# Performance work log

Hardware: AMD Instinct MI355X
Metric: run time of the kernel (lower is better)

The kernel has to match this reference:

```python
import jax, jax.numpy as jnp
import numpy as np

WEIGHT_STD = 0.1
WEIGHT_STD2 = 2.0 * WEIGHT_STD ** 2  # 0.02
CONF_THRESH = 0.9


def setup_inputs() -> dict:
    key = jax.random.key(0)
    k0, k1, k2, k3 = jax.random.split(key, 4)
    B, N, V, J = 1, 32768, 10475, 55
    # skinning weights: nonnegative, rows sum to 1 (as in SMPL-X)
    lbs_weights = jax.random.uniform(k0, (V, J), dtype=jnp.float32)
    lbs_weights = lbs_weights / jnp.sum(lbs_weights, -1, keepdims=True)
    verts_transform = jax.random.normal(k1, (B, V, 4, 4), dtype=jnp.float32)
    points = jax.random.normal(k2, (B, N, 3), dtype=jnp.float32)
    template_points = jax.random.normal(k3, (B, V, 3), dtype=jnp.float32)
    return {
        "lbs_weights": lbs_weights,
        "verts_transform": verts_transform,
        "points": points,
        "template_points": template_points,
        "K": 6,
    }


def _knn(points, template_points, K):
    """Brute-force KNN; squared L2 dists like pytorch3d knn_points. -> dists, idx [B,N,K] ascending."""
    p2 = jnp.sum(points * points, -1)[:, :, None]            # [B,N,1]
    t2 = jnp.sum(template_points * template_points, -1)[:, None, :]  # [B,1,V]
    cross = jnp.einsum("bnd,bvd->bnv", points, template_points)     # [B,N,V]
    d2 = jnp.maximum(p2 + t2 - 2.0 * cross, 0.0)
    neg_d, idx = jax.lax.top_k(-d2, K)  # largest of -d2 == smallest d2, sorted ascending
    return -neg_d, idx


def reference(lbs_weights, verts_transform, points, template_points, K):
    B = points.shape[0]
    neighbs_dist, neighbs = _knn(points, template_points, K)  # [B,N,K]

    # gather skinning weights of the K neighbors: [B,N,K,J]
    w_n = lbs_weights[neighbs]
    # confidence: neighbors whose lbs weights agree with the nearest one
    conf = jnp.exp(-jnp.sum(jnp.abs(w_n - w_n[..., 0:1, :]), -1) / WEIGHT_STD2)
    conf = (conf > CONF_THRESH).astype(neighbs_dist.dtype)
    w = jnp.exp(-neighbs_dist) * conf
    w = w / jnp.sum(w, -1, keepdims=True)  # [B,N,K]; k=0 conf always 1 -> sum > 0

    # gather per-vertex 4x4 transforms: [B,N,K,4,4]
    vt_n = verts_transform[jnp.arange(B)[:, None, None], neighbs]
    xyz_transform = jnp.sum(w[..., None, None] * vt_n, axis=2)   # [B,N,4,4]
    xyz_dist = jnp.sum(w * neighbs_dist, axis=2, keepdims=True)  # [B,N,1]
    return xyz_dist, xyz_transform
```

## Files before the change

### kernel.cpp

```cpp
#include <hip/hip_runtime.h>
#include <math.h>

#pragma clang fp contract(off)

#define NPTS  32768
#define NV    10475
#define JW    55
#define TILE  512
#define NT    21
#define NINIT 10
#define BLOCK 256
#define R     4
#define PPB   16
#define CAP   64
#define FINF  3.4e38f
#define GMARG 0.001f

#define FOR4(M) M(0) M(1) M(2) M(3)

#define LTL(dd, vv, D, I) ((dd) < (D) || ((dd) == (D) && (vv) < (I)))
#define INSL6(dd, vv, D0,I0,D1,I1,D2,I2,D3,I3,D4,I4,D5,I5) \
  if (LTL(dd, vv, D5, I5)) { \
    if (LTL(dd, vv, D4, I4)) { D5=D4; I5=I4; \
      if (LTL(dd, vv, D3, I3)) { D4=D3; I4=I3; \
        if (LTL(dd, vv, D2, I2)) { D3=D2; I3=I2; \
          if (LTL(dd, vv, D1, I1)) { D2=D1; I2=I1; \
            if (LTL(dd, vv, D0, I0)) { D1=D0; I1=I0; D0=(dd); I0=(vv); } \
            else { D1=(dd); I1=(vv); } \
          } else { D2=(dd); I2=(vv); } \
        } else { D3=(dd); I3=(vv); } \
      } else { D4=(dd); I4=(vv); } \
    } else { D5=(dd); I5=(vv); } \
  }

__global__ __launch_bounds__(BLOCK, 6)
void scarf_knn_lbs(const float* __restrict__ lbs,
                   const float* __restrict__ vtf,
                   const float* __restrict__ pts,
                   const float* __restrict__ tpl,
                   float* __restrict__ out_dist,
                   float* __restrict__ out_tf)
{
    __shared__ float4 s_tile[2][TILE];
    __shared__ float  s_bd[PPB][CAP];
    __shared__ int    s_bi[PPB][CAP];
    __shared__ int    s_cnt[PPB];
    __shared__ float  s_td[PPB][6];
    __shared__ int    s_ti[PPB][6];

    const int tid = threadIdx.x;
    const int h   = tid & 63;
    const int w   = tid >> 6;
    const int lp  = w * R;
    const int p0  = blockIdx.x * PPB + lp;

    if (tid < PPB) s_cnt[tid] = 0;

    #define DECLP(r) \
      const float Px##r = 2.0f * pts[(p0+(r))*3+0]; \
      const float Py##r = 2.0f * pts[(p0+(r))*3+1]; \
      const float Pz##r = 2.0f * pts[(p0+(r))*3+2]; \
      const float q##r  = (Px##r*Px##r + Py##r*Py##r) + Pz##r*Pz##r;
    FOR4(DECLP)

    float gx[2], gy[2], gz[2];
    #define STAGE_ISSUE(t_) { \
      _Pragma("unroll") \
      for (int k = 0; k < 2; ++k) { \
        const int j = (t_) * TILE + k * BLOCK + tid; \
        if (j < NV) { gx[k] = tpl[j*3+0]; gy[k] = tpl[j*3+1]; gz[k] = tpl[j*3+2]; } \
        else        { gx[k] = 1.0e6f;    gy[k] = 1.0e6f;    gz[k] = 1.0e6f;    } } }
    #define STAGE_WRITE(dst_) { \
      _Pragma("unroll") \
      for (int k = 0; k < 2; ++k) { \
        const float X = gx[k]+gx[k], Y = gy[k]+gy[k], Z = gz[k]+gz[k]; \
        s_tile[dst_][k * BLOCK + tid] = \
          make_float4(-(X+X), -(Y+Y), -(Z+Z), (X*X + Y*Y) + Z*Z); } }

    #define DECLM(r) float m##r = FINF;
    FOR4(DECLM)

    #define EVP1(r) { \
      const float da = fmaf(Pz##r, ta.z, fmaf(Py##r, ta.y, fmaf(Px##r, ta.x, ta.w))); \
      const float db = fmaf(Pz##r, tb.z, fmaf(Py##r, tb.y, fmaf(Px##r, tb.x, tb.w))); \
      m##r = fminf(fminf(m##r, da), db); }

    STAGE_ISSUE(0); STAGE_WRITE(0); __syncthreads();
    for (int t = 0; t < NINIT; ++t) {
        if (t + 1 < NINIT) STAGE_ISSUE(t + 1);
        const float4* bp = s_tile[t & 1];
        #pragma unroll
        for (int itp = 0; itp < 4; ++itp) {
            const float4 ta = bp[(2*itp    ) * 64 + h];
            const float4 tb = bp[(2*itp + 1) * 64 + h];
            FOR4(EVP1)
        }
        if (t + 1 < NINIT) { STAGE_WRITE((t + 1) & 1); __syncthreads(); }
    }

    #define DECLT(r) float G##r; { \
      float v = m##r; float M; \
      _Pragma("unroll") \
      for (int rep = 0; rep < 6; ++rep) { \
        M = v; \
        M = fminf(M, __shfl_xor(M, 1)); \
        M = fminf(M, __shfl_xor(M, 2)); \
        M = fminf(M, __shfl_xor(M, 4)); \
        M = fminf(M, __shfl_xor(M, 8)); \
        M = fminf(M, __shfl_xor(M, 16)); \
        M = fminf(M, __shfl_xor(M, 32)); \
        if (rep < 5) v = (v == M) ? FINF : v; \
      } \
      G##r = M + GMARG; }
    FOR4(DECLT)

    __syncthreads();

    #define EVP2(r) { \
      const float dp = fmaf(Pz##r, tv.z, fmaf(Py##r, tv.y, fmaf(Px##r, tv.x, tv.w))); \
      if (dp <= G##r) { \
        const float Xr = -0.5f * tv.x, Yr = -0.5f * tv.y, Zr = -0.5f * tv.z; \
        const float C  = fmaf(Pz##r, Zr, fmaf(Py##r, Yr, Px##r * Xr)); \
        const float de = fmaf(-2.0f, C, q##r + tv.w);   \
        const int k = atomicAdd(&s_cnt[lp+(r)], 1); \
        if (k < CAP) { s_bd[lp+(r)][k] = fmaxf(de, 0.0f); s_bi[lp+(r)][k] = tb + it*64 + h; } } }

    STAGE_ISSUE(0); STAGE_WRITE(0); __syncthreads();
    for (int t = 0; t < NT; ++t) {
        if (t + 1 < NT) STAGE_ISSUE(t + 1);
        const float4* bp = s_tile[t & 1];
        const int tb = t * TILE;
        #pragma unroll
        for (int it = 0; it < 8; ++it) {
            const float4 tv = bp[it * 64 + h];
            FOR4(EVP2)
        }
        if (t + 1 < NT) { STAGE_WRITE((t + 1) & 1); __syncthreads(); }
    }

    if (h < R) {
        const int lpr = lp + h;
        float D0=FINF,D1=FINF,D2=FINF,D3=FINF,D4=FINF,D5=FINF;
        int   I0=-1,I1=-1,I2=-1,I3=-1,I4=-1,I5=-1;
        const int cc = s_cnt[lpr];
        const int c  = (cc < CAP) ? cc : CAP;
        for (int k = 0; k < c; ++k) {
            const float dd = s_bd[lpr][k]; const int vv = s_bi[lpr][k];
            INSL6(dd, vv, D0,I0,D1,I1,D2,I2,D3,I3,D4,I4,D5,I5);
        }
        s_td[lpr][0]=D0; s_td[lpr][1]=D1; s_td[lpr][2]=D2;
        s_td[lpr][3]=D3; s_td[lpr][4]=D4; s_td[lpr][5]=D5;
        s_ti[lpr][0]=I0; s_ti[lpr][1]=I1; s_ti[lpr][2]=I2;
        s_ti[lpr][3]=I3; s_ti[lpr][4]=I4; s_ti[lpr][5]=I5;
    }

    const int r  = h >> 4;
    const int l  = h & 15;
    const int lpr = lp + r;
    const int i0 = s_ti[lpr][0];
    const int i1 = s_ti[lpr][1], i2 = s_ti[lpr][2], i3 = s_ti[lpr][3];
    const int i4 = s_ti[lpr][4], i5 = s_ti[lpr][5];
    {
        float s1 = 0.0f, s2 = 0.0f, s3 = 0.0f, s4 = 0.0f, s5 = 0.0f;
        for (int j = l; j < JW; j += 16) {
            const float w0 = lbs[(long)i0 * JW + j];
            s1 += fabsf(lbs[(long)i1 * JW + j] - w0);
            s2 += fabsf(lbs[(long)i2 * JW + j] - w0);
            s3 += fabsf(lbs[(long)i3 * JW + j] - w0);
            s4 += fabsf(lbs[(long)i4 * JW + j] - w0);
            s5 += fabsf(lbs[(long)i5 * JW + j] - w0);
        }
        s1 += __shfl_xor(s1,1); s1 += __shfl_xor(s1,2); s1 += __shfl_xor(s1,4); s1 += __shfl_xor(s1,8);
        s2 += __shfl_xor(s2,1); s2 += __shfl_xor(s2,2); s2 += __shfl_xor(s2,4); s2 += __shfl_xor(s2,8);
        s3 += __shfl_xor(s3,1); s3 += __shfl_xor(s3,2); s3 += __shfl_xor(s3,4); s3 += __shfl_xor(s3,8);
        s4 += __shfl_xor(s4,1); s4 += __shfl_xor(s4,2); s4 += __shfl_xor(s4,4); s4 += __shfl_xor(s4,8);
        s5 += __shfl_xor(s5,1); s5 += __shfl_xor(s5,2); s5 += __shfl_xor(s5,4); s5 += __shfl_xor(s5,8);
        const float sv = (l==0)?s1:(l==1)?s2:(l==2)?s3:(l==3)?s4:s5;
        const bool pred = (l < 5) && (expf(-sv / 0.02f) > 0.9f);
        const unsigned long long bal = __ballot(pred);
        const unsigned mr = (unsigned)(bal >> (r * 16)) & 31u;

        const int P = p0 + r;
        const float d0 = 0.25f * s_td[lpr][0], d1 = 0.25f * s_td[lpr][1];
        const float d2 = 0.25f * s_td[lpr][2], d3 = 0.25f * s_td[lpr][3];
        const float d4 = 0.25f * s_td[lpr][4], d5 = 0.25f * s_td[lpr][5];

        const float w0 = expf(-d0);
        const float w1 = (mr & 1u)  ? expf(-d1) : 0.0f;
        const float w2 = (mr & 2u)  ? expf(-d2) : 0.0f;
        const float w3 = (mr & 4u)  ? expf(-d3) : 0.0f;
        const float w4 = (mr & 8u)  ? expf(-d4) : 0.0f;
        const float w5 = (mr & 16u) ? expf(-d5) : 0.0f;
        const float inv = 1.0f / (w0 + w1 + w2 + w3 + w4 + w5);
        const float n0 = w0*inv, n1 = w1*inv, n2 = w2*inv;
        const float n3 = w3*inv, n4 = w4*inv, n5 = w5*inv;

        if (l == 0)
            out_dist[P] = n0*d0 + n1*d1 + n2*d2 + n3*d3 + n4*d4 + n5*d5;

        float acc = n0 * vtf[i0*16 + l];
        acc = fmaf(n1, vtf[i1*16 + l], acc);
        acc = fmaf(n2, vtf[i2*16 + l], acc);
        acc = fmaf(n3, vtf[i3*16 + l], acc);
        acc = fmaf(n4, vtf[i4*16 + l], acc);
        acc = fmaf(n5, vtf[i5*16 + l], acc);
        out_tf[P*16 + l] = acc;
    }
}

extern "C" void kernel_launch(void* const* d_in, const int* in_sizes, int n_in,
                              void* d_out, int out_size, void* d_ws, size_t ws_size,
                              hipStream_t stream) {
    const float* lbs = (const float*)d_in[0];
    const float* vtf = (const float*)d_in[1];
    const float* pts = (const float*)d_in[2];
    const float* tpl = (const float*)d_in[3];
    float* out = (float*)d_out;
    scarf_knn_lbs<<<NPTS / PPB, BLOCK, 0, stream>>>(lbs, vtf, pts, tpl, out, out + NPTS);
}
```

Before: 121.1 us.

## Store only candidate indices in LDS, recompute distances in selection, shuffle results

```diff
diff --git a/kernel.cpp b/kernel.cpp
--- a/kernel.cpp
+++ b/kernel.cpp
@@ -12,7 +12,7 @@
 #define BLOCK 256
 #define R     4
 #define PPB   16
-#define CAP   64
+#define CAP   60
 #define FINF  3.4e38f
 #define GMARG 0.001f
 
@@ -33,7 +33,7 @@
     } else { D5=(dd); I5=(vv); } \
   }
 
-__global__ __launch_bounds__(BLOCK, 6)
+__global__ __launch_bounds__(BLOCK, 8)
 void scarf_knn_lbs(const float* __restrict__ lbs,
                    const float* __restrict__ vtf,
                    const float* __restrict__ pts,
@@ -42,11 +42,7 @@
                    float* __restrict__ out_tf)
 {
     __shared__ float4 s_tile[2][TILE];
-    __shared__ float  s_bd[PPB][CAP];
-    __shared__ int    s_bi[PPB][CAP];
-    __shared__ int    s_cnt[PPB];
-    __shared__ float  s_td[PPB][6];
-    __shared__ int    s_ti[PPB][6];
+    __shared__ int    s_bi[PPB][CAP + 1];
 
     const int tid = threadIdx.x;
     const int h   = tid & 63;
@@ -54,7 +50,7 @@
     const int lp  = w * R;
     const int p0  = blockIdx.x * PPB + lp;
 
-    if (tid < PPB) s_cnt[tid] = 0;
+    if (tid < PPB) s_bi[tid][CAP] = 0;
 
     #define DECLP(r) \
       const float Px##r = 2.0f * pts[(p0+(r))*3+0]; \
@@ -119,11 +115,8 @@
     #define EVP2(r) { \
       const float dp = fmaf(Pz##r, tv.z, fmaf(Py##r, tv.y, fmaf(Px##r, tv.x, tv.w))); \
       if (dp <= G##r) { \
-        const float Xr = -0.5f * tv.x, Yr = -0.5f * tv.y, Zr = -0.5f * tv.z; \
-        const float C  = fmaf(Pz##r, Zr, fmaf(Py##r, Yr, Px##r * Xr)); \
-        const float de = fmaf(-2.0f, C, q##r + tv.w);   \
-        const int k = atomicAdd(&s_cnt[lp+(r)], 1); \
-        if (k < CAP) { s_bd[lp+(r)][k] = fmaxf(de, 0.0f); s_bi[lp+(r)][k] = tb + it*64 + h; } } }
+        const int k = atomicAdd(&s_bi[lp+(r)][CAP], 1); \
+        if (k < CAP) s_bi[lp+(r)][k] = tb + it*64 + h; } }
 
     STAGE_ISSUE(0); STAGE_WRITE(0); __syncthreads();
     for (int t = 0; t < NT; ++t) {
@@ -138,28 +131,35 @@
         if (t + 1 < NT) { STAGE_WRITE((t + 1) & 1); __syncthreads(); }
     }
 
+    float D0=FINF,D1=FINF,D2=FINF,D3=FINF,D4=FINF,D5=FINF;
+    int   I0=-1,I1=-1,I2=-1,I3=-1,I4=-1,I5=-1;
     if (h < R) {
         const int lpr = lp + h;
-        float D0=FINF,D1=FINF,D2=FINF,D3=FINF,D4=FINF,D5=FINF;
-        int   I0=-1,I1=-1,I2=-1,I3=-1,I4=-1,I5=-1;
-        const int cc = s_cnt[lpr];
+        const float Phx = (h==0)?Px0:(h==1)?Px1:(h==2)?Px2:Px3;
+        const float Phy = (h==0)?Py0:(h==1)?Py1:(h==2)?Py2:Py3;
+        const float Phz = (h==0)?Pz0:(h==1)?Pz1:(h==2)?Pz2:Pz3;
+        const float qh  = (h==0)?q0 :(h==1)?q1 :(h==2)?q2 :q3;
+        const int cc = s_bi[lpr][CAP];
         const int c  = (cc < CAP) ? cc : CAP;
         for (int k = 0; k < c; ++k) {
-            const float dd = s_bd[lpr][k]; const int vv = s_bi[lpr][k];
-            INSL6(dd, vv, D0,I0,D1,I1,D2,I2,D3,I3,D4,I4,D5,I5);
-        }
-        s_td[lpr][0]=D0; s_td[lpr][1]=D1; s_td[lpr][2]=D2;
-        s_td[lpr][3]=D3; s_td[lpr][4]=D4; s_td[lpr][5]=D5;
-        s_ti[lpr][0]=I0; s_ti[lpr][1]=I1; s_ti[lpr][2]=I2;
-        s_ti[lpr][3]=I3; s_ti[lpr][4]=I4; s_ti[lpr][5]=I5;
+            const int vv = s_bi[lpr][k];
+            const float tx = tpl[vv*3+0], ty = tpl[vv*3+1], tz = tpl[vv*3+2];
+            const float X = tx+tx, Y = ty+ty, Z = tz+tz;
+            const float t2 = (X*X + Y*Y) + Z*Z;
+            const float C  = fmaf(Phz, Z, fmaf(Phy, Y, Phx * X));
+            const float de = fmaxf(fmaf(-2.0f, C, qh + t2), 0.0f);
+            INSL6(de, vv, D0,I0,D1,I1,D2,I2,D3,I3,D4,I4,D5,I5);
+        }
     }
 
     const int r  = h >> 4;
     const int l  = h & 15;
-    const int lpr = lp + r;
-    const int i0 = s_ti[lpr][0];
-    const int i1 = s_ti[lpr][1], i2 = s_ti[lpr][2], i3 = s_ti[lpr][3];
-    const int i4 = s_ti[lpr][4], i5 = s_ti[lpr][5];
+    const int i0 = __shfl(I0, r), i1 = __shfl(I1, r), i2 = __shfl(I2, r);
+    const int i3 = __shfl(I3, r), i4 = __shfl(I4, r), i5 = __shfl(I5, r);
+    const float d0 = 0.25f * __shfl(D0, r), d1 = 0.25f * __shfl(D1, r);
+    const float d2 = 0.25f * __shfl(D2, r), d3 = 0.25f * __shfl(D3, r);
+    const float d4 = 0.25f * __shfl(D4, r), d5 = 0.25f * __shfl(D5, r);
+
     {
         float s1 = 0.0f, s2 = 0.0f, s3 = 0.0f, s4 = 0.0f, s5 = 0.0f;
         for (int j = l; j < JW; j += 16) {
@@ -181,10 +181,6 @@
         const unsigned mr = (unsigned)(bal >> (r * 16)) & 31u;
 
         const int P = p0 + r;
-        const float d0 = 0.25f * s_td[lpr][0], d1 = 0.25f * s_td[lpr][1];
-        const float d2 = 0.25f * s_td[lpr][2], d3 = 0.25f * s_td[lpr][3];
-        const float d4 = 0.25f * s_td[lpr][4], d5 = 0.25f * s_td[lpr][5];
-
         const float w0 = expf(-d0);
         const float w1 = (mr & 1u)  ? expf(-d1) : 0.0f;
         const float w2 = (mr & 2u)  ? expf(-d2) : 0.0f;
```

After: 104.3 us. 13.9% less time.
